# Performance work log

Measured on AMD Instinct MI355X. Metric: run time of the kernel, lower is better.

## Reference

```python
import jax, jax.numpy as jnp
import numpy as np

D = 128   # hidden_size
L = 50    # mailbox length (USER_MAX_LEN / ITEM_MAX_LEN)
NU = 8192 # num user nodes
NI = 8192 # num item nodes


def setup_inputs() -> dict:
    key = jax.random.key(0)
    ks = jax.random.split(key, 16)
    s = 0.05
    return {
        "user": jax.random.normal(ks[0], (NU, D), jnp.float32),
        "item": jax.random.normal(ks[1], (NI, D), jnp.float32),
        "W_user": jax.random.normal(ks[2], (D, D), jnp.float32) * s,
        "W_item": jax.random.normal(ks[3], (D, D), jnp.float32) * s,
        "agg_gate_user": jax.random.normal(ks[4], (2 * D, D), jnp.float32) * s,
        "agg_gate_item": jax.random.normal(ks[5], (2 * D, D), jnp.float32) * s,
        "update_user": jax.random.normal(ks[6], (2 * D, D), jnp.float32) * s,
        "update_item": jax.random.normal(ks[7], (2 * D, D), jnp.float32) * s,
        "user_date_emb": jax.random.normal(ks[8], (L, D), jnp.float32) * s,
        "user_date_emb_k": jax.random.normal(ks[9], (L, D), jnp.float32) * s,
        "item_date_emb": jax.random.normal(ks[10], (L, D), jnp.float32) * s,
        "item_date_emb_k": jax.random.normal(ks[11], (L, D), jnp.float32) * s,
        "user_nbr": jax.random.randint(ks[12], (NU, L), 0, NI, jnp.int64) if jax.config.jax_enable_x64 else jax.random.randint(ks[12], (NU, L), 0, NI, jnp.int32),
        "user_nbr_time": jax.random.randint(ks[13], (NU, L), 0, 1000000, jnp.int32),
        "item_nbr": jax.random.randint(ks[14], (NI, L), 0, NU, jnp.int32),
        "item_nbr_time": jax.random.randint(ks[15], (NI, L), 0, 1000000, jnp.int32),
    }


def _reduce(dst_h, src_mail, time, emb, emb_k, gate_W):
    # dst_h: [N,d], src_mail: [N,L,d], time: [N,L]
    # double argsort -> rank; reorder = L - rank - 1 (time-order position)
    order = jnp.argsort(jnp.argsort(time, axis=1), axis=1)
    reorder = time.shape[1] - order - 1                     # [N,L]
    scale = 1.0 / jnp.sqrt(jnp.asarray(dst_h.shape[-1], dst_h.dtype))
    # long-term attention with positional injection
    e = jnp.sum((emb[reorder] + src_mail) * dst_h[:, None, :], axis=-1) * scale
    alpha = jax.nn.softmax(e, axis=1)                       # [N,L]
    h_long = jnp.einsum('nl,nld->nd', alpha, src_mail + emb_k[reorder])
    # short-term attention against most-recent neighbor
    last = jnp.argmax(time, axis=1)                         # [N]
    last_emb = jnp.take_along_axis(src_mail, last[:, None, None], axis=1)  # [N,1,d]
    e1 = jnp.sum(last_emb * src_mail, axis=-1) * scale
    alpha1 = jax.nn.softmax(e1, axis=1)
    h_short = jnp.einsum('nl,nld->nd', alpha1, src_mail)
    return jnp.concatenate([h_long, h_short], axis=-1) @ gate_W  # [N,d]


def reference(user, item, W_user, W_item, agg_gate_user, agg_gate_item,
              update_user, update_item, user_date_emb, user_date_emb_k,
              item_date_emb, item_date_emb_k, user_nbr, user_nbr_time,
              item_nbr, item_nbr_time):
    # feat_drop/attn_drop are identity (eval mode)
    uh = user @ W_user   # [NU,d]
    ih = item @ W_item   # [NI,d]
    # user nodes aggregate item-neighbor mailboxes
    user_agg = _reduce(uh, ih[user_nbr], user_nbr_time,
                       user_date_emb, user_date_emb_k, agg_gate_user)
    # item nodes aggregate user-neighbor mailboxes
    item_agg = _reduce(ih, uh[item_nbr], item_nbr_time,
                       item_date_emb, item_date_emb_k, agg_gate_item)
    user_out = jnp.tanh(jnp.concatenate([user_agg, user], axis=-1) @ update_user)
    item_out = jnp.tanh(jnp.concatenate([item_agg, item], axis=-1) @ update_item)
    return user_out, item_out
```

## Files before the change

### kernel.cpp

```cpp
#include <hip/hip_runtime.h>
#include <math.h>

#define D 128
#define L 50
#define SCALE 0.08838834764831845f

using bf16x8 = __attribute__((ext_vector_type(8))) short;
using f32x4  = __attribute__((ext_vector_type(4))) float;

union FragU { bf16x8 f; uint2 u2[2]; };

__device__ __forceinline__ unsigned f2bf(float x) {
    union { float f; unsigned u; } v; v.f = x;
    return (v.u + 0x7fffu + ((v.u >> 16) & 1u)) >> 16;
}
__device__ __forceinline__ float bflo(unsigned u) {
    union { unsigned u; float f; } v; v.u = u << 16; return v.f;
}
__device__ __forceinline__ float bfhi(unsigned u) {
    union { unsigned u; float f; } v; v.u = u & 0xffff0000u; return v.f;
}

__global__ __launch_bounds__(256) void prep_all_kernel(
    const float* __restrict__ Wu, const float* __restrict__ Wi,
    const float* __restrict__ ue, const float* __restrict__ ie,
    const float* __restrict__ gu, const float* __restrict__ gi,
    const float* __restrict__ uu, const float* __restrict__ ui,
    const float* __restrict__ uek, const float* __restrict__ iek,
    unsigned short* __restrict__ Bptu, unsigned short* __restrict__ Bpti,
    unsigned short* __restrict__ Btu, unsigned short* __restrict__ Bti)
{
    __shared__ float T[2][128];
    int b = blockIdx.x, t = threadIdx.x;
    if (b < 50) {
        int side = b / 25;
        int o = (b % 25) * 256 + t;
        int d = o / L, l = o % L;
        const float* W = side ? Wi : Wu;
        const float* E = side ? ie : ue;
        unsigned short* Bpt = side ? Bpti : Bptu;
        float a = 0.f;
        for (int k = 0; k < D; ++k) a += W[d * D + k] * E[l * D + k];
        Bpt[(128 + l) * 128 + d] = (unsigned short)f2bf(a);
    } else if (b < 306) {
        int bb = b - 50;
        int side = bb / 128;
        int o = (bb % 128) * 256 + t;
        int r = o >> 7, c = o & 127;
        const float* G = side ? gi : gu;
        const float* U = side ? ui : uu;
        unsigned short* Bt = side ? Bti : Btu;
        float a = 0.f;
        for (int k = 0; k < D; ++k) a += G[r * D + k] * U[k * D + c];
        Bt[c * 448 + r] = (unsigned short)f2bf(a);
    } else if (b < 434) {
        int bb = b - 306;
        int side = bb >> 6;
        int o = (bb & 63) * 256 + t;
        int r = o >> 7, c = o & 127;
        const float* U = side ? ui : uu;
        unsigned short* Bt = side ? Bti : Btu;
        Bt[c * 448 + 320 + r] = (unsigned short)f2bf(U[(128 + r) * D + c]);
        if (r < 14) Bt[c * 448 + 306 + r] = 0;
    } else if (b < 562) {
        int bb = b - 434;
        int side = bb >> 6;
        int o = (bb & 63) * 256 + t;
        int k = o >> 7, c = o & 127;
        const float* W = side ? Wi : Wu;
        unsigned short* Bpt = side ? Bpti : Bptu;
        Bpt[c * 128 + k] = (unsigned short)f2bf(W[k * D + c]);
    } else if (b < 564) {
        int side = b - 562;
        unsigned short* Bpt = side ? Bpti : Bptu;
        for (int j = 0; j < 7; ++j)
            Bpt[178 * 128 + t * 7 + j] = 0;
    } else {
        int bb = b - 564;
        int side = bb / 25;
        int ro = (bb % 25) * 2;
        const float* EK = side ? iek : uek;
        const float* G  = side ? gi : gu;
        const float* U  = side ? ui : uu;
        unsigned short* Bt = side ? Bti : Btu;
        int r = t >> 7, c = t & 127;
        float a = 0.f;
        for (int k = 0; k < D; ++k) a += EK[(ro + r) * D + k] * G[k * D + c];
        T[r][c] = a;
        __syncthreads();
        float e = 0.f;
        for (int j = 0; j < D; ++j) e += T[r][j] * U[j * D + c];
        Bt[c * 448 + 256 + ro + r] = (unsigned short)f2bf(e);
    }
}

__global__ __launch_bounds__(256) void proj_mfma(
    const float* __restrict__ Xu, const float* __restrict__ Xi,
    const unsigned* __restrict__ Bptu32, const unsigned* __restrict__ Bpti32,
    unsigned* __restrict__ h32, float* __restrict__ eproj,
    unsigned* __restrict__ A32, int NU)
{
    __shared__ __align__(16) unsigned As[32 * 20];
    __shared__ __align__(16) unsigned Bs[192 * 20];
    int t = threadIdx.x;
    int nb = blockIdx.x * 32;
    const float* X = (nb < NU) ? Xu : Xi;
    int xoff = (nb < NU) ? 0 : NU;
    const unsigned* Bt = (nb < NU) ? Bptu32 : Bpti32;
    int wave = t >> 6, lane = t & 63;
    int m16 = lane & 15, quad = lane >> 4;

    f32x4 acc[2][3];
    for (int i = 0; i < 2; ++i)
        for (int j = 0; j < 3; ++j) acc[i][j] = (f32x4){0.f, 0.f, 0.f, 0.f};

    for (int kc = 0; kc < 4; ++kc) {
        if (t < 128) {
            int row = t >> 2, q = t & 3;
            int n = nb + row;
            const float* src = &X[(size_t)(n - xoff) * D + kc * 32 + q * 8];
            float4 v0 = *(const float4*)&src[0];
            float4 v1 = *(const float4*)&src[4];
            uint4 pk;
            pk.x = f2bf(v0.x) | (f2bf(v0.y) << 16);
            pk.y = f2bf(v0.z) | (f2bf(v0.w) << 16);
            pk.z = f2bf(v1.x) | (f2bf(v1.y) << 16);
            pk.w = f2bf(v1.z) | (f2bf(v1.w) << 16);
            *(uint4*)&As[row * 20 + q * 4] = pk;
            *(uint4*)&A32[(size_t)n * 224 + 160 + kc * 16 + q * 4] = pk;
        }
        #pragma unroll
        for (int i = 0; i < 3; ++i) {
            int idx = t * 3 + i;
            int c = idx >> 2, q = idx & 3;
            uint4 v = *(const uint4*)&Bt[(size_t)c * 64 + kc * 16 + q * 4];
            *(uint4*)&Bs[c * 20 + q * 4] = v;
        }
        __syncthreads();
        bf16x8 a0 = *(const bf16x8*)&As[m16 * 20 + quad * 4];
        bf16x8 a1 = *(const bf16x8*)&As[(16 + m16) * 20 + quad * 4];
        #pragma unroll
        for (int ni = 0; ni < 3; ++ni) {
            bf16x8 bb = *(const bf16x8*)&Bs[(wave * 48 + ni * 16 + m16) * 20 + quad * 4];
            acc[0][ni] = __builtin_amdgcn_mfma_f32_16x16x32_bf16(a0, bb, acc[0][ni], 0, 0, 0);
            acc[1][ni] = __builtin_amdgcn_mfma_f32_16x16x32_bf16(a1, bb, acc[1][ni], 0, 0, 0);
        }
        __syncthreads();
    }
    #pragma unroll
    for (int mi = 0; mi < 2; ++mi)
        #pragma unroll
        for (int ni = 0; ni < 3; ++ni) {
            int col = wave * 48 + ni * 16 + m16;
            #pragma unroll
            for (int r = 0; r < 4; ++r) {
                float me = acc[mi][ni][r];
                float pr = __shfl_xor(me, 1);
                int row = nb + mi * 16 + quad * 4 + r;
                if (col < 128) {
                    if (!(lane & 1))
                        h32[(size_t)row * 64 + (col >> 1)] = f2bf(me) | (f2bf(pr) << 16);
                } else if (col < 178) {
                    eproj[(size_t)row * L + (col - 128)] = me;
                }
            }
        }
}

__global__ __launch_bounds__(256) void agg_kernel(
    const unsigned* __restrict__ h32, const float* __restrict__ eproj,
    const int* __restrict__ unbr, const int* __restrict__ untime,
    const int* __restrict__ inbr, const int* __restrict__ intime,
    unsigned* __restrict__ A32, int NU, int NI)
{
    __shared__ unsigned smail[2][L * 66];
    __shared__ unsigned shb[2][64];
    __shared__ float se2[2][2][64];
    __shared__ float salpha[2][L], salpha1[2][L];
    __shared__ int stime[2][L], sreorder[2][L], snbr[2][L], slast[2];

    int tb = threadIdx.x;
    int sub = tb >> 7;
    int t = tb & 127;
    int g = blockIdx.x * 2 + sub;
    int wave = t >> 6, lane = t & 63;
    int m16 = lane & 15, quad = lane >> 4;

    const unsigned* mail; const int* nbrp; const int* timp;
    if (g < NU) { mail = h32 + (size_t)NU * 64; nbrp = unbr + (size_t)g * L;        timp = untime + (size_t)g * L; }
    else        { mail = h32;                   nbrp = inbr + (size_t)(g - NU) * L; timp = intime + (size_t)(g - NU) * L; }

    if (t < 64) shb[sub][t] = h32[(size_t)g * 64 + t];
    if (t < L) { stime[sub][t] = timp[t]; snbr[sub][t] = nbrp[t]; }
    __syncthreads();

    if (t < L) {
        int ti = stime[sub][t]; int rank = 0; bool firstmax = true;
        for (int j = 0; j < L; ++j) {
            int tj = stime[sub][j];
            rank += (tj < ti) || (tj == ti && j < t);
            firstmax = firstmax && ((tj < ti) || (tj == ti && j >= t));
        }
        sreorder[sub][t] = L - 1 - rank;
        if (firstmax) slast[sub] = t;
    }
    {
        int q = t >> 5, p = t & 31;
        #pragma unroll
        for (int i = 0; i < 13; ++i) {
            int l = i * 4 + q;
            if (l < L) {
                uint2 v = *(const uint2*)&mail[(size_t)snbr[sub][l] * 64 + p * 2];
                *(uint2*)&smail[sub][l * 66 + 2 * p] = v;
            }
        }
    }
    __syncthreads();

    {
        const unsigned* bptr = (m16 == 1) ? &smail[sub][slast[sub] * 66]
                                          : &shb[sub][0];
        int s0 = wave * 32 + m16;  if (s0 > 49) s0 = 49;
        int s1 = wave * 32 + 16 + m16;  if (s1 > 49) s1 = 49;
        const unsigned* a0p = &smail[sub][s0 * 66];
        const unsigned* a1p = &smail[sub][s1 * 66];
        f32x4 d0 = {0.f, 0.f, 0.f, 0.f}, d1 = {0.f, 0.f, 0.f, 0.f};
        #pragma unroll
        for (int kc = 0; kc < 4; ++kc) {
            int off = kc * 16 + quad * 4;
            FragU bf_, af0, af1;
            bf_.u2[0] = *(const uint2*)&bptr[off];
            bf_.u2[1] = *(const uint2*)&bptr[off + 2];
            af0.u2[0] = *(const uint2*)&a0p[off];
            af0.u2[1] = *(const uint2*)&a0p[off + 2];
            af1.u2[0] = *(const uint2*)&a1p[off];
            af1.u2[1] = *(const uint2*)&a1p[off + 2];
            d0 = __builtin_amdgcn_mfma_f32_16x16x32_bf16(af0.f, bf_.f, d0, 0, 0, 0);
            d1 = __builtin_amdgcn_mfma_f32_16x16x32_bf16(af1.f, bf_.f, d1, 0, 0, 0);
        }
        if (m16 < 2) {
            #pragma unroll
            for (int r = 0; r < 4; ++r) {
                se2[sub][m16][wave * 32 + quad * 4 + r]      = d0[r];
                se2[sub][m16][wave * 32 + 16 + quad * 4 + r] = d1[r];
            }
        }
    }
    __syncthreads();

    float sc = -1e30f;
    if (lane < L) {
        sc = (wave == 0)
           ? (se2[sub][0][lane] + eproj[(size_t)g * L + sreorder[sub][lane]]) * SCALE
           : se2[sub][1][lane] * SCALE;
    }
    float mx = sc;
    for (int off = 32; off; off >>= 1) mx = fmaxf(mx, __shfl_xor(mx, off));
    float ex = (lane < L) ? expf(sc - mx) : 0.f;
    float sm = ex;
    for (int off = 32; off; off >>= 1) sm += __shfl_xor(sm, off);
    float al = ex / sm;
    if (lane < L) { if (wave == 0) salpha[sub][lane] = al; else salpha1[sub][lane] = al; }
    __syncthreads();

    {
        const float* alp = wave ? salpha1[sub] : salpha[sub];
        const unsigned* base = &smail[sub][lane];
        float ax = 0.f, ay = 0.f;
        for (int l = 0; l < L; ++l) {
            unsigned u = base[l * 66];
            float a = alp[l];
            ax += a * bflo(u);
            ay += a * bfhi(u);
        }
        A32[(size_t)g * 224 + wave * 64 + lane] = f2bf(ax) | (f2bf(ay) << 16);
    }
    if (t >= 64 && t < 96) A32[(size_t)g * 224 + 128 + (t - 64)] = 0u;
    __syncthreads();
    if (t < L) {
        ((unsigned short*)A32)[(size_t)g * 448 + 256 + sreorder[sub][t]] =
            (unsigned short)f2bf(salpha[sub][t]);
    }
}

__global__ __launch_bounds__(256) void gemm_out_mfma(
    const unsigned* __restrict__ A32,
    const unsigned* __restrict__ Btu32, const unsigned* __restrict__ Bti32,
    float* __restrict__ out, int NU)
{
    __shared__ __align__(16) unsigned As[32 * 20];
    __shared__ __align__(16) unsigned Bs[128 * 20];
    int t = threadIdx.x;
    int nb = blockIdx.x * 32;
    const unsigned* Bt = (nb < NU) ? Btu32 : Bti32;
    int wave = t >> 6, lane = t & 63;
    int m16 = lane & 15, quad = lane >> 4;
    int ncol0 = wave * 32;

    f32x4 acc[2][2] = {{{0.f, 0.f, 0.f, 0.f}, {0.f, 0.f, 0.f, 0.f}},
                       {{0.f, 0.f, 0.f, 0.f}, {0.f, 0.f, 0.f, 0.f}}};

    for (int kc = 0; kc < 14; ++kc) {
        if (t < 128) {
            int row = t >> 2, q = t & 3;
            uint4 v = *(const uint4*)&A32[(size_t)(nb + row) * 224 + kc * 16 + q * 4];
            *(uint4*)&As[row * 20 + q * 4] = v;
        }
        #pragma unroll
        for (int i = 0; i < 2; ++i) {
            int idx = t * 2 + i;
            int n = idx >> 2, q = idx & 3;
            uint4 v = *(const uint4*)&Bt[(size_t)n * 224 + kc * 16 + q * 4];
            *(uint4*)&Bs[n * 20 + q * 4] = v;
        }
        __syncthreads();
        bf16x8 a0 = *(const bf16x8*)&As[m16 * 20 + quad * 4];
        bf16x8 a1 = *(const bf16x8*)&As[(16 + m16) * 20 + quad * 4];
        bf16x8 b0 = *(const bf16x8*)&Bs[(ncol0 + m16) * 20 + quad * 4];
        bf16x8 b1 = *(const bf16x8*)&Bs[(ncol0 + 16 + m16) * 20 + quad * 4];
        acc[0][0] = __builtin_amdgcn_mfma_f32_16x16x32_bf16(a0, b0, acc[0][0], 0, 0, 0);
        acc[0][1] = __builtin_amdgcn_mfma_f32_16x16x32_bf16(a0, b1, acc[0][1], 0, 0, 0);
        acc[1][0] = __builtin_amdgcn_mfma_f32_16x16x32_bf16(a1, b0, acc[1][0], 0, 0, 0);
        acc[1][1] = __builtin_amdgcn_mfma_f32_16x16x32_bf16(a1, b1, acc[1][1], 0, 0, 0);
        __syncthreads();
    }
    #pragma unroll
    for (int mi = 0; mi < 2; ++mi)
        #pragma unroll
        for (int ni = 0; ni < 2; ++ni)
            #pragma unroll
            for (int r = 0; r < 4; ++r) {
                int row = nb + mi * 16 + quad * 4 + r;
                int col = ncol0 + ni * 16 + m16;
                out[(size_t)row * D + col] = tanhf(acc[mi][ni][r]);
            }
}

extern "C" void kernel_launch(void* const* d_in, const int* in_sizes, int n_in,
                              void* d_out, int out_size, void* d_ws, size_t ws_size,
                              hipStream_t stream) {
    const float* user   = (const float*)d_in[0];
    const float* item   = (const float*)d_in[1];
    const float* Wu     = (const float*)d_in[2];
    const float* Wi     = (const float*)d_in[3];
    const float* gate_u = (const float*)d_in[4];
    const float* gate_i = (const float*)d_in[5];
    const float* upd_u  = (const float*)d_in[6];
    const float* upd_i  = (const float*)d_in[7];
    const float* uemb   = (const float*)d_in[8];
    const float* uembk  = (const float*)d_in[9];
    const float* iemb   = (const float*)d_in[10];
    const float* iembk  = (const float*)d_in[11];
    const int*   unbr   = (const int*)d_in[12];
    const int*   untime = (const int*)d_in[13];
    const int*   inbr   = (const int*)d_in[14];
    const int*   intime = (const int*)d_in[15];

    int NU = in_sizes[0] / D;
    int NI = in_sizes[1] / D;
    int N  = NU + NI;

    float* eproj  = (float*)d_ws;
    unsigned* h32   = (unsigned*)(eproj + (size_t)N * L);
    unsigned* A32   = h32 + (size_t)N * 64;
    unsigned* Btu32 = A32 + (size_t)N * 224;
    unsigned* Bti32 = Btu32 + 128 * 224;
    unsigned* Bptu32 = Bti32 + 128 * 224;
    unsigned* Bpti32 = Bptu32 + 192 * 64;

    prep_all_kernel<<<614, 256, 0, stream>>>(Wu, Wi, uemb, iemb, gate_u, gate_i,
                                             upd_u, upd_i, uembk, iembk,
                                             (unsigned short*)Bptu32,
                                             (unsigned short*)Bpti32,
                                             (unsigned short*)Btu32,
                                             (unsigned short*)Bti32);
    proj_mfma<<<N / 32, 256, 0, stream>>>(user, item, Bptu32, Bpti32,
                                          h32, eproj, A32, NU);
    agg_kernel<<<N / 2, 256, 0, stream>>>(h32, eproj, unbr, untime, inbr,
                                          intime, A32, NU, NI);
    gemm_out_mfma<<<N / 32, 256, 0, stream>>>(A32, Btu32, Bti32,
                                              (float*)d_out, NU);
}
```

Before: 173.7 us.

## Preload full B operand into LDS once and load A fragments directly in GEMMs

Both projection and output GEMMs now stage the whole B matrix into LDS once per block and drop the per-k-chunk A staging and double barriers. A fragments are read straight from global memory into registers. The output GEMM is re-tiled so each block covers 128 rows by 64 columns, halving the grid. This trades larger LDS use (about 58 KB in the output GEMM) and lower occupancy for fewer barriers and less redundant B traffic.

```diff
diff --git a/kernel.cpp b/kernel.cpp
--- a/kernel.cpp
+++ b/kernel.cpp
@@ -8,7 +8,7 @@
 using bf16x8 = __attribute__((ext_vector_type(8))) short;
 using f32x4  = __attribute__((ext_vector_type(4))) float;
 
-union FragU { bf16x8 f; uint2 u2[2]; };
+union FragU { bf16x8 f; uint2 u2[2]; uint4 u4; };
 
 __device__ __forceinline__ unsigned f2bf(float x) {
     union { float f; unsigned u; } v; v.f = x;
@@ -100,8 +100,7 @@
     unsigned* __restrict__ h32, float* __restrict__ eproj,
     unsigned* __restrict__ A32, int NU)
 {
-    __shared__ __align__(16) unsigned As[32 * 20];
-    __shared__ __align__(16) unsigned Bs[192 * 20];
+    __shared__ __align__(16) unsigned Bs[192 * 68];
     int t = threadIdx.x;
     int nb = blockIdx.x * 32;
     const float* X = (nb < NU) ? Xu : Xi;
@@ -110,15 +109,26 @@
     int wave = t >> 6, lane = t & 63;
     int m16 = lane & 15, quad = lane >> 4;
 
+    #pragma unroll
+    for (int i = 0; i < 12; ++i) {
+        int idx = t + i * 256;
+        int c = idx >> 4, q = idx & 15;
+        uint4 v = *(const uint4*)&Bt[(size_t)c * 64 + q * 4];
+        *(uint4*)&Bs[c * 68 + q * 4] = v;
+    }
+    __syncthreads();
+
     f32x4 acc[2][3];
     for (int i = 0; i < 2; ++i)
         for (int j = 0; j < 3; ++j) acc[i][j] = (f32x4){0.f, 0.f, 0.f, 0.f};
 
+    #pragma unroll
     for (int kc = 0; kc < 4; ++kc) {
-        if (t < 128) {
-            int row = t >> 2, q = t & 3;
-            int n = nb + row;
-            const float* src = &X[(size_t)(n - xoff) * D + kc * 32 + q * 8];
+        FragU a[2];
+        #pragma unroll
+        for (int mi = 0; mi < 2; ++mi) {
+            int row = nb + mi * 16 + m16;
+            const float* src = &X[(size_t)(row - xoff) * D + kc * 32 + quad * 8];
             float4 v0 = *(const float4*)&src[0];
             float4 v1 = *(const float4*)&src[4];
             uint4 pk;
@@ -126,26 +136,16 @@
             pk.y = f2bf(v0.z) | (f2bf(v0.w) << 16);
             pk.z = f2bf(v1.x) | (f2bf(v1.y) << 16);
             pk.w = f2bf(v1.z) | (f2bf(v1.w) << 16);
-            *(uint4*)&As[row * 20 + q * 4] = pk;
-            *(uint4*)&A32[(size_t)n * 224 + 160 + kc * 16 + q * 4] = pk;
-        }
-        #pragma unroll
-        for (int i = 0; i < 3; ++i) {
-            int idx = t * 3 + i;
-            int c = idx >> 2, q = idx & 3;
-            uint4 v = *(const uint4*)&Bt[(size_t)c * 64 + kc * 16 + q * 4];
-            *(uint4*)&Bs[c * 20 + q * 4] = v;
-        }
-        __syncthreads();
-        bf16x8 a0 = *(const bf16x8*)&As[m16 * 20 + quad * 4];
-        bf16x8 a1 = *(const bf16x8*)&As[(16 + m16) * 20 + quad * 4];
+            a[mi].u4 = pk;
+            if (wave == 0)
+                *(uint4*)&A32[(size_t)row * 224 + 160 + kc * 16 + quad * 4] = pk;
+        }
         #pragma unroll
         for (int ni = 0; ni < 3; ++ni) {
-            bf16x8 bb = *(const bf16x8*)&Bs[(wave * 48 + ni * 16 + m16) * 20 + quad * 4];
-            acc[0][ni] = __builtin_amdgcn_mfma_f32_16x16x32_bf16(a0, bb, acc[0][ni], 0, 0, 0);
-            acc[1][ni] = __builtin_amdgcn_mfma_f32_16x16x32_bf16(a1, bb, acc[1][ni], 0, 0, 0);
-        }
-        __syncthreads();
+            bf16x8 bb = *(const bf16x8*)&Bs[(wave * 48 + ni * 16 + m16) * 68 + kc * 16 + quad * 4];
+            acc[0][ni] = __builtin_amdgcn_mfma_f32_16x16x32_bf16(a[0].f, bb, acc[0][ni], 0, 0, 0);
+            acc[1][ni] = __builtin_amdgcn_mfma_f32_16x16x32_bf16(a[1].f, bb, acc[1][ni], 0, 0, 0);
+        }
     }
     #pragma unroll
     for (int mi = 0; mi < 2; ++mi)
@@ -288,52 +288,46 @@
     const unsigned* __restrict__ Btu32, const unsigned* __restrict__ Bti32,
     float* __restrict__ out, int NU)
 {
-    __shared__ __align__(16) unsigned As[32 * 20];
-    __shared__ __align__(16) unsigned Bs[128 * 20];
+    __shared__ __align__(16) unsigned Bs[64 * 228];
     int t = threadIdx.x;
-    int nb = blockIdx.x * 32;
+    int rowblk = blockIdx.x >> 1, half = blockIdx.x & 1;
+    int nb = rowblk * 128;
     const unsigned* Bt = (nb < NU) ? Btu32 : Bti32;
     int wave = t >> 6, lane = t & 63;
     int m16 = lane & 15, quad = lane >> 4;
-    int ncol0 = wave * 32;
-
-    f32x4 acc[2][2] = {{{0.f, 0.f, 0.f, 0.f}, {0.f, 0.f, 0.f, 0.f}},
-                       {{0.f, 0.f, 0.f, 0.f}, {0.f, 0.f, 0.f, 0.f}}};
-
-    for (int kc = 0; kc < 14; ++kc) {
-        if (t < 128) {
-            int row = t >> 2, q = t & 3;
-            uint4 v = *(const uint4*)&A32[(size_t)(nb + row) * 224 + kc * 16 + q * 4];
-            *(uint4*)&As[row * 20 + q * 4] = v;
-        }
-        #pragma unroll
-        for (int i = 0; i < 2; ++i) {
-            int idx = t * 2 + i;
-            int n = idx >> 2, q = idx & 3;
-            uint4 v = *(const uint4*)&Bt[(size_t)n * 224 + kc * 16 + q * 4];
-            *(uint4*)&Bs[n * 20 + q * 4] = v;
-        }
-        __syncthreads();
-        bf16x8 a0 = *(const bf16x8*)&As[m16 * 20 + quad * 4];
-        bf16x8 a1 = *(const bf16x8*)&As[(16 + m16) * 20 + quad * 4];
-        bf16x8 b0 = *(const bf16x8*)&Bs[(ncol0 + m16) * 20 + quad * 4];
-        bf16x8 b1 = *(const bf16x8*)&Bs[(ncol0 + 16 + m16) * 20 + quad * 4];
-        acc[0][0] = __builtin_amdgcn_mfma_f32_16x16x32_bf16(a0, b0, acc[0][0], 0, 0, 0);
-        acc[0][1] = __builtin_amdgcn_mfma_f32_16x16x32_bf16(a0, b1, acc[0][1], 0, 0, 0);
-        acc[1][0] = __builtin_amdgcn_mfma_f32_16x16x32_bf16(a1, b0, acc[1][0], 0, 0, 0);
-        acc[1][1] = __builtin_amdgcn_mfma_f32_16x16x32_bf16(a1, b1, acc[1][1], 0, 0, 0);
-        __syncthreads();
-    }
-    #pragma unroll
-    for (int mi = 0; mi < 2; ++mi)
-        #pragma unroll
-        for (int ni = 0; ni < 2; ++ni)
+
+    #pragma unroll
+    for (int i = 0; i < 14; ++i) {
+        int idx = t + i * 256;
+        int n = idx / 56, q = idx - n * 56;
+        uint4 v = *(const uint4*)&Bt[(size_t)(half * 64 + n) * 224 + q * 4];
+        *(uint4*)&Bs[n * 228 + q * 4] = v;
+    }
+    __syncthreads();
+
+    #pragma unroll
+    for (int j = 0; j < 2; ++j) {
+        int mrow0 = nb + (wave * 2 + j) * 16;
+        f32x4 acc[4] = {{0.f,0.f,0.f,0.f},{0.f,0.f,0.f,0.f},
+                        {0.f,0.f,0.f,0.f},{0.f,0.f,0.f,0.f}};
+        for (int kc = 0; kc < 14; ++kc) {
+            FragU af;
+            af.u4 = *(const uint4*)&A32[(size_t)(mrow0 + m16) * 224 + kc * 16 + quad * 4];
+            #pragma unroll
+            for (int ni = 0; ni < 4; ++ni) {
+                bf16x8 bf = *(const bf16x8*)&Bs[(ni * 16 + m16) * 228 + kc * 16 + quad * 4];
+                acc[ni] = __builtin_amdgcn_mfma_f32_16x16x32_bf16(af.f, bf, acc[ni], 0, 0, 0);
+            }
+        }
+        #pragma unroll
+        for (int ni = 0; ni < 4; ++ni)
             #pragma unroll
             for (int r = 0; r < 4; ++r) {
-                int row = nb + mi * 16 + quad * 4 + r;
-                int col = ncol0 + ni * 16 + m16;
-                out[(size_t)row * D + col] = tanhf(acc[mi][ni][r]);
-            }
+                int row = mrow0 + quad * 4 + r;
+                int col = half * 64 + ni * 16 + m16;
+                out[(size_t)row * D + col] = tanhf(acc[ni][r]);
+            }
+    }
 }
 
 extern "C" void kernel_launch(void* const* d_in, const int* in_sizes, int n_in,
@@ -378,6 +372,6 @@
                                           h32, eproj, A32, NU);
     agg_kernel<<<N / 2, 256, 0, stream>>>(h32, eproj, unbr, untime, inbr,
                                           intime, A32, NU, NI);
-    gemm_out_mfma<<<N / 32, 256, 0, stream>>>(A32, Btu32, Bti32,
+    gemm_out_mfma<<<N / 64, 256, 0, stream>>>(A32, Btu32, Bti32,
                                               (float*)d_out, NU);
 }
```

Result: no change. 172.1 us (-0.9%).
